# Kernel optimization log

Measured on AMD Instinct MI355X. Metric: run time of the kernel, lower is better.

The kernel has to match this reference:

```python
import jax, jax.numpy as jnp
import numpy as np
import math

B, S, D, H, KVH = 4, 2048, 4096, 32, 8
HD = D // H          # 128
N_REP = H // KVH     # 4
MAX_S = 2048


def setup_inputs() -> dict:
    key = jax.random.key(0)
    ks = jax.random.split(key, 6)
    x = jax.random.normal(ks[0], (B, S, D), dtype=jnp.float32)
    sc = 0.02
    wq = jax.random.normal(ks[1], (D, H * HD), dtype=jnp.float32) * sc
    wk = jax.random.normal(ks[2], (D, KVH * HD), dtype=jnp.float32) * sc
    wv = jax.random.normal(ks[3], (D, KVH * HD), dtype=jnp.float32) * sc
    wo = jax.random.normal(ks[4], (H * HD, D), dtype=jnp.float32) * sc
    # RoPE tables (matches llama precompute_freqs_cis, theta=10000)
    inv_freq = 1.0 / (10000.0 ** (np.arange(0, HD, 2, dtype=np.float32) / HD))  # [HD/2]
    t = np.arange(S, dtype=np.float32)
    freqs = np.outer(t, inv_freq)  # [S, HD/2]
    cos = jnp.asarray(np.cos(freqs), dtype=jnp.float32)
    sin = jnp.asarray(np.sin(freqs), dtype=jnp.float32)
    cache_k = jnp.zeros((B, MAX_S, KVH, HD), dtype=jnp.float32)
    cache_v = jnp.zeros((B, MAX_S, KVH, HD), dtype=jnp.float32)
    return {"x": x, "wq": wq, "wk": wk, "wv": wv, "wo": wo,
            "cos": cos, "sin": sin, "cache_k": cache_k, "cache_v": cache_v,
            "start_pos": 0}


def _apply_rope(x, cos, sin):
    # x: [B, S, h, HD]; interleaved complex rotation, as torch view_as_complex
    xr = x.reshape(*x.shape[:-1], HD // 2, 2)
    x0, x1 = xr[..., 0], xr[..., 1]
    c = cos[None, :, None, :]
    s = sin[None, :, None, :]
    o0 = x0 * c - x1 * s
    o1 = x0 * s + x1 * c
    return jnp.stack([o0, o1], axis=-1).reshape(x.shape)


def reference(x, wq, wk, wv, wo, cos, sin, cache_k, cache_v, start_pos):
    bsz, seqlen, _ = x.shape
    xq = (x @ wq).reshape(bsz, seqlen, H, HD)
    xk = (x @ wk).reshape(bsz, seqlen, KVH, HD)
    xv = (x @ wv).reshape(bsz, seqlen, KVH, HD)
    xq = _apply_rope(xq, cos, sin)
    xk = _apply_rope(xk, cos, sin)
    # KV cache update then slice [:start_pos+seqlen]
    cache_k = jax.lax.dynamic_update_slice(cache_k, xk, (0, start_pos, 0, 0))
    cache_v = jax.lax.dynamic_update_slice(cache_v, xv, (0, start_pos, 0, 0))
    kv_len = start_pos + seqlen
    keys = cache_k[:, :kv_len]    # [B, K, KVH, HD]
    values = cache_v[:, :kv_len]
    # repeat_kv: expand kv heads by n_rep (GQA)
    keys = jnp.repeat(keys, N_REP, axis=2)      # [B, K, H, HD]
    values = jnp.repeat(values, N_REP, axis=2)
    scores = jnp.einsum('bqhd,bkhd->bhqk', xq, keys) / math.sqrt(HD)
    probs = jax.nn.softmax(scores.astype(jnp.float32), axis=-1).astype(xq.dtype)
    out = jnp.einsum('bhqk,bkhd->bqhd', probs, values)
    out = out.reshape(bsz, seqlen, H * HD)
    return out @ wo
```

## Files before the change

kernel.cpp:

```cpp
#include <hip/hip_runtime.h>
#include <math.h>
#include <stdint.h>

typedef unsigned short u16;
typedef __attribute__((ext_vector_type(8))) short short8;
typedef __attribute__((ext_vector_type(4))) float f32x4;

#define B_   4
#define S_   2048
#define D_   4096
#define H_   32
#define KVH_ 8
#define HD_  128
#define NQKV 6144
#define MTOT 8192
#define ATT_SCALE 0.08838834764831845f

__device__ __forceinline__ float bf2f(u16 u) {
  unsigned x = ((unsigned)u) << 16;
  return __builtin_bit_cast(float, x);
}
__device__ __forceinline__ u16 f2bf(float f) {
  unsigned x = __builtin_bit_cast(unsigned, f);
  x += 0x7fffu + ((x >> 16) & 1u);
  return (u16)(x >> 16);
}
__device__ __forceinline__ unsigned pack2bf(float a, float b) {
  return (unsigned)f2bf(a) | ((unsigned)f2bf(b) << 16);
}

typedef const __attribute__((address_space(1))) void* gas1p;
typedef __attribute__((address_space(3))) void* las3p;
__device__ __forceinline__ void gload16(const void* g, void* l) {
  __builtin_amdgcn_global_load_lds((gas1p)g, (las3p)l, 16, 0, 0);
}

__device__ __forceinline__ int swz64(int row, int kc) {
  return row * 64 + ((kc ^ (row & 7)) << 3);
}
__device__ __forceinline__ int swz128(int row, int kc) {
  return row * 128 + ((kc ^ (row & 7)) << 3);
}

__global__ void cast_f32_to_bf16(const float* __restrict__ in, u16* __restrict__ out, long n) {
  long i = ((long)blockIdx.x * 256 + threadIdx.x) * 4;
  if (i >= n) return;
  float4 v = *(const float4*)(in + i);
  ushort4 o;
  o.x = f2bf(v.x); o.y = f2bf(v.y); o.z = f2bf(v.z); o.w = f2bf(v.w);
  *(ushort4*)(out + i) = o;
}

__global__ void transpose_cast(const float* __restrict__ in, u16* __restrict__ out, int K, int N) {
  __shared__ u16 tile[32][33];
  int n0 = blockIdx.x * 32, k0 = blockIdx.y * 32;
  int tx = threadIdx.x, ty = threadIdx.y;
  for (int i = ty; i < 32; i += 8)
    tile[i][tx] = f2bf(in[(long)(k0 + i) * N + n0 + tx]);
  __syncthreads();
  for (int i = ty; i < 32; i += 8)
    out[(long)(n0 + i) * K + k0 + tx] = tile[tx][i];
}

template <int OUTF32>
__global__ __launch_bounds__(512, 2) void gemm256(const u16* __restrict__ A,
                                                  const u16* __restrict__ BT,
                                                  void* __restrict__ Cout,
                                                  int M, int N, int K) {
  __shared__ u16 Ls[2][2][2][128 * 64];
  int tid = threadIdx.x, lane = tid & 63, wid = tid >> 6;
  int wm = wid >> 2, wn = wid & 3;
  int m0 = blockIdx.y * 256, n0 = blockIdx.x * 256;
  int frow = lane & 15, fk = lane >> 4;

  f32x4 acc[8][4];
#pragma unroll
  for (int i = 0; i < 8; i++)
#pragma unroll
    for (int j = 0; j < 4; j++) acc[i][j] = (f32x4){0.f, 0.f, 0.f, 0.f};

  int srow = lane >> 3;
  int sc = ((lane & 7) ^ srow) * 8;
  const u16* a0 = A + (long)(m0 + (2 * wid + 0) * 8 + srow) * K + sc;
  const u16* a1 = A + (long)(m0 + (2 * wid + 1) * 8 + srow) * K + sc;
  const u16* b0 = BT + (long)(n0 + (2 * wid + 0) * 8 + srow) * K + sc;
  const u16* b1 = BT + (long)(n0 + (2 * wid + 1) * 8 + srow) * K + sc;
  long hstep = (long)128 * K;

#define STAGE_A(buf, half, t) do {                                              \
    gload16(a0 + (half) * hstep + (long)(t) * 64, &Ls[buf][0][half][(2 * wid + 0) * 512]); \
    gload16(a1 + (half) * hstep + (long)(t) * 64, &Ls[buf][0][half][(2 * wid + 1) * 512]); \
  } while (0)
#define STAGE_B(buf, half, t) do {                                              \
    gload16(b0 + (half) * hstep + (long)(t) * 64, &Ls[buf][1][half][(2 * wid + 0) * 512]); \
    gload16(b1 + (half) * hstep + (long)(t) * 64, &Ls[buf][1][half][(2 * wid + 1) * 512]); \
  } while (0)

  int nk = K / 64;
  STAGE_A(0, 0, 0); STAGE_A(0, 1, 0); STAGE_B(0, 0, 0); STAGE_B(0, 1, 0);
  STAGE_B(1, 0, 1); STAGE_B(1, 1, 1);
  asm volatile("s_waitcnt vmcnt(4)" ::: "memory");
  __builtin_amdgcn_s_barrier();

#define PHASE(P, STAGE_STMT, VM_STMT)                                           \
  {                                                                             \
    short8 af[2][2];                                                            \
    _Pragma("unroll") for (int mm = 0; mm < 2; mm++)                            \
      _Pragma("unroll") for (int kk = 0; kk < 2; kk++)                          \
        af[mm][kk] = *(const short8*)&Ah[swz64((2 * (P) + mm) * 16 + frow, kk * 4 + fk)]; \
    STAGE_STMT;                                                                 \
    VM_STMT;                                                                    \
    __builtin_amdgcn_s_barrier();                                               \
    asm volatile("s_waitcnt lgkmcnt(0)" ::: "memory");                          \
    __builtin_amdgcn_sched_barrier(0);                                          \
    __builtin_amdgcn_s_setprio(1);                                              \
    _Pragma("unroll") for (int mm = 0; mm < 2; mm++)                            \
      _Pragma("unroll") for (int n = 0; n < 4; n++)                             \
        _Pragma("unroll") for (int kk = 0; kk < 2; kk++)                        \
          acc[2 * (P) + mm][n] = __builtin_amdgcn_mfma_f32_16x16x32_bf16(       \
              af[mm][kk], bfr[n][kk], acc[2 * (P) + mm][n], 0, 0, 0);           \
    __builtin_amdgcn_s_setprio(0);                                              \
    __builtin_amdgcn_s_barrier();                                               \
  }

  for (int t = 0; t < nk; ++t) {
    int pi = t & 1;
    const u16* Ah = &Ls[pi][0][wm][0];
    const u16* Bh = &Ls[pi][1][wn >> 1][0];
    int brow = (wn & 1) * 64;
    short8 bfr[4][2];
#pragma unroll
    for (int n = 0; n < 4; n++)
#pragma unroll
      for (int kk = 0; kk < 2; kk++)
        bfr[n][kk] = *(const short8*)&Bh[swz64(brow + n * 16 + frow, kk * 4 + fk)];

    PHASE(0, if (t + 1 < nk) STAGE_A(pi ^ 1, 0, t + 1), );
    PHASE(1, if (t + 1 < nk) STAGE_A(pi ^ 1, 1, t + 1), );
    PHASE(2, if (t + 2 < nk) STAGE_B(pi, 0, t + 2), );
    PHASE(3, if (t + 2 < nk) STAGE_B(pi, 1, t + 2),
          if (t + 2 < nk) { asm volatile("s_waitcnt vmcnt(4)" ::: "memory"); }
          else            { asm volatile("s_waitcnt vmcnt(0)" ::: "memory"); });
  }
#undef PHASE
#undef STAGE_A
#undef STAGE_B

  int cc = lane & 15, cr = fk * 4;
#pragma unroll
  for (int i = 0; i < 8; i++)
#pragma unroll
    for (int j = 0; j < 4; j++)
#pragma unroll
      for (int r = 0; r < 4; r++) {
        int m = m0 + wm * 128 + i * 16 + cr + r;
        int n = n0 + wn * 64 + j * 16 + cc;
        if (OUTF32)
          ((float*)Cout)[(long)m * N + n] = acc[i][j][r];
        else
          ((u16*)Cout)[(long)m * N + n] = f2bf(acc[i][j][r]);
      }
}

__global__ void rope_kernel(u16* __restrict__ qkv, const float* __restrict__ cosb,
                            const float* __restrict__ sinb, const int* __restrict__ start_pos) {
  long tid = (long)blockIdx.x * 256 + threadIdx.x;
  const long total = (long)MTOT * 2560;
  if (tid >= total) return;
  int row = (int)(tid / 2560);
  int p = (int)(tid % 2560);
  int col = (p < 2048) ? (p * 2) : (D_ + (p - 2048) * 2);
  int i = (col >> 1) & 63;
  int s = row & (S_ - 1);
  int pos = s + *start_pos;
  float c = cosb[pos * 64 + i];
  float sn = sinb[pos * 64 + i];
  u16* ptr = qkv + (long)row * NQKV + col;
  unsigned v = *(unsigned*)ptr;
  float x0 = bf2f((u16)(v & 0xffff));
  float x1 = bf2f((u16)(v >> 16));
  float o0 = x0 * c - x1 * sn;
  float o1 = x0 * sn + x1 * c;
  unsigned ov = (unsigned)f2bf(o0) | ((unsigned)f2bf(o1) << 16);
  *(unsigned*)ptr = ov;
}

__global__ void build_vt(const u16* __restrict__ qkv, u16* __restrict__ vt) {
  int bk = blockIdx.z;
  int b = bk >> 3, kvh = bk & 7;
  int s0 = blockIdx.x * 32, d0 = blockIdx.y * 32;
  __shared__ u16 tile[32][33];
  int tx = threadIdx.x, ty = threadIdx.y;
  const u16* src = qkv + (long)(b * S_) * NQKV + D_ + KVH_ * HD_ + kvh * HD_;
  for (int i = ty; i < 32; i += 8)
    tile[i][tx] = src[(long)(s0 + i) * NQKV + d0 + tx];
  __syncthreads();
  u16* dst = vt + ((long)(b * KVH_ + kvh) * HD_) * S_;
  for (int i = ty; i < 32; i += 8)
    dst[(long)(d0 + i) * S_ + s0 + tx] = tile[tx][i];
}

__global__ __launch_bounds__(256, 3) void attn_kernel(const u16* __restrict__ qkv,
                                                      const u16* __restrict__ vt,
                                                      u16* __restrict__ obuf) {
  int nb = gridDim.x;
  int fid = (int)((blockIdx.x & 7) * (nb >> 3) + (blockIdx.x >> 3));
  int bx = fid & 15;
  int bh = fid >> 4;
  int b = bh >> 5, h = bh & 31;
  int kvh = h >> 2;
  int q0 = bx * 128;
  int tid = threadIdx.x, lane = tid & 63, wid = tid >> 6;

  __shared__ u16 Ks[64 * 128];
  __shared__ u16 VTs[128 * 64];
  __shared__ u16 Ps[4][32 * 64];

  int frow = lane & 15;
  int fk = lane >> 4;

  short8 qf[2][4];
#pragma unroll
  for (int qq = 0; qq < 2; ++qq) {
    const u16* qbase = qkv + (long)(b * S_ + q0 + wid * 32 + qq * 16 + frow) * NQKV + h * HD_;
#pragma unroll
    for (int kd = 0; kd < 4; ++kd) qf[qq][kd] = *(const short8*)(qbase + kd * 32 + fk * 8);
  }

  f32x4 acc_o[2][8];
#pragma unroll
  for (int qq = 0; qq < 2; qq++)
#pragma unroll
    for (int i = 0; i < 8; i++) acc_o[qq][i] = (f32x4){0.f, 0.f, 0.f, 0.f};
  float m_r[2] = {-1e30f, -1e30f};
  float l_r[2] = {0.f, 0.f};

  const u16* kgl[4];
  const u16* vgl[4];
#pragma unroll
  for (int j = 0; j < 4; j++) {
    int gk = j * 4 + wid;
    int rk = gk * 4 + (lane >> 4);
    int ck = (lane & 15) ^ (rk & 7);
    kgl[j] = qkv + (long)(b * S_ + rk) * NQKV + D_ + kvh * HD_ + ck * 8;
    int gv = j * 4 + wid;
    int rv = gv * 8 + (lane >> 3);
    int cv = (lane & 7) ^ (rv & 7);
    vgl[j] = vt + ((long)(b * KVH_ + kvh) * HD_ + rv) * S_ + cv * 8;
  }

  const int ntiles = S_ / 64;
  for (int t = 0; t < ntiles; ++t) {
#pragma unroll
    for (int j = 0; j < 4; j++) {
      int g = j * 4 + wid;
      gload16(kgl[j] + (long)(t * 64) * NQKV, &Ks[g * 512]);
      gload16(vgl[j] + t * 64, &VTs[g * 512]);
    }
    __syncthreads();

    f32x4 sc[4][2];
#pragma unroll
    for (int f = 0; f < 4; f++)
#pragma unroll
      for (int qq = 0; qq < 2; qq++) sc[f][qq] = (f32x4){0.f, 0.f, 0.f, 0.f};
#pragma unroll
    for (int f = 0; f < 4; f++)
#pragma unroll
      for (int kd = 0; kd < 4; kd++) {
        short8 kf = *(const short8*)&Ks[swz128(f * 16 + frow, kd * 4 + fk)];
        sc[f][0] = __builtin_amdgcn_mfma_f32_16x16x32_bf16(kf, qf[0][kd], sc[f][0], 0, 0, 0);
        sc[f][1] = __builtin_amdgcn_mfma_f32_16x16x32_bf16(kf, qf[1][kd], sc[f][1], 0, 0, 0);
      }

#pragma unroll
    for (int qq = 0; qq < 2; ++qq) {
      float mx = sc[0][qq][0];
#pragma unroll
      for (int f = 0; f < 4; f++)
#pragma unroll
        for (int r = 0; r < 4; r++) mx = fmaxf(mx, sc[f][qq][r]);
      mx = fmaxf(mx, __shfl_xor(mx, 16, 64));
      mx = fmaxf(mx, __shfl_xor(mx, 32, 64));
      float mnew = fmaxf(m_r[qq], mx);
      float scl = __expf((m_r[qq] - mnew) * ATT_SCALE);
      float nms = -mnew * ATT_SCALE;
      float rs = 0.f;
      int prow = qq * 16 + frow;
      int pbase = prow * 64 + (fk & 1) * 4;
      int q7 = frow & 7;
#pragma unroll
      for (int f = 0; f < 4; f++) {
        float p0 = __expf(fmaf(sc[f][qq][0], ATT_SCALE, nms));
        float p1 = __expf(fmaf(sc[f][qq][1], ATT_SCALE, nms));
        float p2 = __expf(fmaf(sc[f][qq][2], ATT_SCALE, nms));
        float p3 = __expf(fmaf(sc[f][qq][3], ATT_SCALE, nms));
        rs += (p0 + p1) + (p2 + p3);
        unsigned lo = pack2bf(p0, p1);
        unsigned hi = pack2bf(p2, p3);
        int chunk = (f * 2 + (fk >> 1)) ^ q7;
        uint2 wv2; wv2.x = lo; wv2.y = hi;
        *(uint2*)&Ps[wid][pbase + (chunk << 3)] = wv2;
      }
      rs += __shfl_xor(rs, 16, 64);
      rs += __shfl_xor(rs, 32, 64);
      l_r[qq] = l_r[qq] * scl + rs;
      m_r[qq] = mnew;
#pragma unroll
      for (int df = 0; df < 8; df++) acc_o[qq][df] *= scl;
    }

    asm volatile("s_waitcnt lgkmcnt(0)" ::: "memory");
    __builtin_amdgcn_sched_barrier(0);

    short8 pf[2][2];
#pragma unroll
    for (int qq = 0; qq < 2; qq++)
#pragma unroll
      for (int kk = 0; kk < 2; kk++)
        pf[qq][kk] = *(const short8*)&Ps[wid][(qq * 16 + frow) * 64 + (((kk * 4 + fk) ^ (frow & 7)) << 3)];
#pragma unroll
    for (int df = 0; df < 8; df++)
#pragma unroll
      for (int kk = 0; kk < 2; kk++) {
        short8 vf = *(const short8*)&VTs[swz64(df * 16 + frow, kk * 4 + fk)];
        acc_o[0][df] = __builtin_amdgcn_mfma_f32_16x16x32_bf16(vf, pf[0][kk], acc_o[0][df], 0, 0, 0);
        acc_o[1][df] = __builtin_amdgcn_mfma_f32_16x16x32_bf16(vf, pf[1][kk], acc_o[1][df], 0, 0, 0);
      }
    __syncthreads();
  }

#pragma unroll
  for (int qq = 0; qq < 2; ++qq) {
    float inv = 1.0f / l_r[qq];
    long srow = (long)(b * S_ + q0 + wid * 32 + qq * 16 + frow);
    u16* orow = obuf + srow * D_ + h * HD_ + fk * 4;
#pragma unroll
    for (int df = 0; df < 8; df++) {
      uint2 ov;
      ov.x = pack2bf(acc_o[qq][df][0] * inv, acc_o[qq][df][1] * inv);
      ov.y = pack2bf(acc_o[qq][df][2] * inv, acc_o[qq][df][3] * inv);
      *(uint2*)(orow + df * 16) = ov;
    }
  }
}

extern "C" void kernel_launch(void* const* d_in, const int* in_sizes, int n_in,
                              void* d_out, int out_size, void* d_ws, size_t ws_size,
                              hipStream_t stream) {
  const float* x = (const float*)d_in[0];
  const float* wq = (const float*)d_in[1];
  const float* wk = (const float*)d_in[2];
  const float* wv = (const float*)d_in[3];
  const float* wo = (const float*)d_in[4];
  const float* cosb = (const float*)d_in[5];
  const float* sinb = (const float*)d_in[6];
  const int* start_pos = (const int*)d_in[9];
  float* out = (float*)d_out;

  char* ws = (char*)d_ws;
  u16* xb = (u16*)ws;
  u16* wqkvT = (u16*)(ws + 67108864L);
  u16* woT = (u16*)(ws + 117440512L);
  u16* qkvb = (u16*)(ws + 150994944L);
  u16* vtb = (u16*)(ws + 251658240L);
  u16* obuf = xb;

  cast_f32_to_bf16<<<dim3(32768), dim3(256), 0, stream>>>(x, xb, (long)MTOT * D_);

  transpose_cast<<<dim3(128, 128), dim3(32, 8), 0, stream>>>(wq, wqkvT, D_, 4096);
  transpose_cast<<<dim3(32, 128), dim3(32, 8), 0, stream>>>(wk, wqkvT + (long)4096 * D_, D_, 1024);
  transpose_cast<<<dim3(32, 128), dim3(32, 8), 0, stream>>>(wv, wqkvT + (long)5120 * D_, D_, 1024);
  transpose_cast<<<dim3(128, 128), dim3(32, 8), 0, stream>>>(wo, woT, D_, 4096);

  gemm256<0><<<dim3(NQKV / 256, MTOT / 256), dim3(512), 0, stream>>>(xb, wqkvT, qkvb, MTOT, NQKV, D_);

  rope_kernel<<<dim3(81920), dim3(256), 0, stream>>>(qkvb, cosb, sinb, start_pos);

  build_vt<<<dim3(64, 4, 32), dim3(32, 8), 0, stream>>>(qkvb, vtb);

  attn_kernel<<<dim3(2048), dim3(256), 0, stream>>>(qkvb, vtb, obuf);

  gemm256<1><<<dim3(D_ / 256, MTOT / 256), dim3(512), 0, stream>>>(obuf, woT, out, MTOT, D_, D_);
}
```

Measured before the change: 1.143 ms.

## Double-buffer K/V tiles in attention and defer online-softmax rescaling

Result: faster. 1.051 ms (-8.1%).

```diff
diff --git a/kernel.cpp b/kernel.cpp
--- a/kernel.cpp
+++ b/kernel.cpp
@@ -15,6 +15,7 @@
 #define NQKV 6144
 #define MTOT 8192
 #define ATT_SCALE 0.08838834764831845f
+#define DEFER_THR 90.5f
 
 __device__ __forceinline__ float bf2f(u16 u) {
   unsigned x = ((unsigned)u) << 16;
@@ -200,7 +201,7 @@
     dst[(long)(d0 + i) * S_ + s0 + tx] = tile[tx][i];
 }
 
-__global__ __launch_bounds__(256, 3) void attn_kernel(const u16* __restrict__ qkv,
+__global__ __launch_bounds__(256, 2) void attn_kernel(const u16* __restrict__ qkv,
                                                       const u16* __restrict__ vt,
                                                       u16* __restrict__ obuf) {
   int nb = gridDim.x;
@@ -212,8 +213,8 @@
   int q0 = bx * 128;
   int tid = threadIdx.x, lane = tid & 63, wid = tid >> 6;
 
-  __shared__ u16 Ks[64 * 128];
-  __shared__ u16 VTs[128 * 64];
+  __shared__ u16 Ks[2][64 * 128];
+  __shared__ u16 VTs[2][128 * 64];
   __shared__ u16 Ps[4][32 * 64];
 
   int frow = lane & 15;
@@ -249,15 +250,28 @@
     vgl[j] = vt + ((long)(b * KVH_ + kvh) * HD_ + rv) * S_ + cv * 8;
   }
 
+#define STAGE_KV(buf, t) do {                                                   \
+    _Pragma("unroll") for (int j = 0; j < 4; j++) {                             \
+      int g = j * 4 + wid;                                                      \
+      gload16(kgl[j] + (long)((t) * 64) * NQKV, &Ks[buf][g * 512]);             \
+      gload16(vgl[j] + (t) * 64, &VTs[buf][g * 512]);                           \
+    }                                                                           \
+  } while (0)
+
   const int ntiles = S_ / 64;
+  STAGE_KV(0, 0);
+
   for (int t = 0; t < ntiles; ++t) {
-#pragma unroll
-    for (int j = 0; j < 4; j++) {
-      int g = j * 4 + wid;
-      gload16(kgl[j] + (long)(t * 64) * NQKV, &Ks[g * 512]);
-      gload16(vgl[j] + t * 64, &VTs[g * 512]);
+    if (t + 1 < ntiles) {
+      STAGE_KV((t + 1) & 1, t + 1);
+      asm volatile("s_waitcnt vmcnt(8)" ::: "memory");
+    } else {
+      asm volatile("s_waitcnt vmcnt(0)" ::: "memory");
     }
-    __syncthreads();
+    __builtin_amdgcn_s_barrier();
+    __builtin_amdgcn_sched_barrier(0);
+    const u16* Kb = &Ks[t & 1][0];
+    const u16* Vb = &VTs[t & 1][0];
 
     f32x4 sc[4][2];
 #pragma unroll
@@ -268,23 +282,38 @@
     for (int f = 0; f < 4; f++)
 #pragma unroll
       for (int kd = 0; kd < 4; kd++) {
-        short8 kf = *(const short8*)&Ks[swz128(f * 16 + frow, kd * 4 + fk)];
+        short8 kf = *(const short8*)&Kb[swz128(f * 16 + frow, kd * 4 + fk)];
         sc[f][0] = __builtin_amdgcn_mfma_f32_16x16x32_bf16(kf, qf[0][kd], sc[f][0], 0, 0, 0);
         sc[f][1] = __builtin_amdgcn_mfma_f32_16x16x32_bf16(kf, qf[1][kd], sc[f][1], 0, 0, 0);
       }
 
+    float mx[2];
 #pragma unroll
     for (int qq = 0; qq < 2; ++qq) {
-      float mx = sc[0][qq][0];
+      float m = sc[0][qq][0];
 #pragma unroll
       for (int f = 0; f < 4; f++)
 #pragma unroll
-        for (int r = 0; r < 4; r++) mx = fmaxf(mx, sc[f][qq][r]);
-      mx = fmaxf(mx, __shfl_xor(mx, 16, 64));
-      mx = fmaxf(mx, __shfl_xor(mx, 32, 64));
-      float mnew = fmaxf(m_r[qq], mx);
-      float scl = __expf((m_r[qq] - mnew) * ATT_SCALE);
-      float nms = -mnew * ATT_SCALE;
+        for (int r = 0; r < 4; r++) m = fmaxf(m, sc[f][qq][r]);
+      m = fmaxf(m, __shfl_xor(m, 16, 64));
+      m = fmaxf(m, __shfl_xor(m, 32, 64));
+      mx[qq] = m;
+    }
+    if (!__all((mx[0] <= m_r[0] + DEFER_THR) && (mx[1] <= m_r[1] + DEFER_THR))) {
+#pragma unroll
+      for (int qq = 0; qq < 2; ++qq) {
+        float mnew = fmaxf(m_r[qq], mx[qq]);
+        float scl = __expf((m_r[qq] - mnew) * ATT_SCALE);
+        l_r[qq] *= scl;
+        m_r[qq] = mnew;
+#pragma unroll
+        for (int df = 0; df < 8; df++) acc_o[qq][df] *= scl;
+      }
+    }
+
+#pragma unroll
+    for (int qq = 0; qq < 2; ++qq) {
+      float nms = -m_r[qq] * ATT_SCALE;
       float rs = 0.f;
       int prow = qq * 16 + frow;
       int pbase = prow * 64 + (fk & 1) * 4;
@@ -304,10 +333,7 @@
       }
       rs += __shfl_xor(rs, 16, 64);
       rs += __shfl_xor(rs, 32, 64);
-      l_r[qq] = l_r[qq] * scl + rs;
-      m_r[qq] = mnew;
-#pragma unroll
-      for (int df = 0; df < 8; df++) acc_o[qq][df] *= scl;
+      l_r[qq] += rs;
     }
 
     asm volatile("s_waitcnt lgkmcnt(0)" ::: "memory");
@@ -323,12 +349,13 @@
     for (int df = 0; df < 8; df++)
 #pragma unroll
       for (int kk = 0; kk < 2; kk++) {
-        short8 vf = *(const short8*)&VTs[swz64(df * 16 + frow, kk * 4 + fk)];
+        short8 vf = *(const short8*)&Vb[swz64(df * 16 + frow, kk * 4 + fk)];
         acc_o[0][df] = __builtin_amdgcn_mfma_f32_16x16x32_bf16(vf, pf[0][kk], acc_o[0][df], 0, 0, 0);
         acc_o[1][df] = __builtin_amdgcn_mfma_f32_16x16x32_bf16(vf, pf[1][kk], acc_o[1][df], 0, 0, 0);
       }
     __syncthreads();
   }
+#undef STAGE_KV
 
 #pragma unroll
   for (int qq = 0; qq < 2; ++qq) {
```
